# Kernel tuning notes

Measured on AMD Instinct MI355X. Metric: run time of the kernel, lower is better.

## Reference

```python
import jax, jax.numpy as jnp
import numpy as np

DIM = 512
HEADS = 8
DH = DIM // HEADS          # 64
M = DIM // 2               # 256 landmarks
PINV_ITERS = 6
KERNEL = 33                # residual_conv_kernel (lucidrains default)
SCALE = DH ** -0.5
LN_EPS = 1e-5


def setup_inputs() -> dict:
    key = jax.random.key(0)
    ks = jax.random.split(key, 6)
    b, n = 4, 4096
    x = jax.random.normal(ks[0], (b, n, DIM), jnp.float32)
    ln_w = jnp.ones((DIM,), jnp.float32)
    ln_b = jnp.zeros((DIM,), jnp.float32)
    w_qkv = jax.random.normal(ks[1], (DIM, 3 * DIM), jnp.float32) / np.float32(np.sqrt(DIM))
    w_out = jax.random.normal(ks[2], (DIM, DIM), jnp.float32) / np.float32(np.sqrt(DIM))
    b_out = jnp.zeros((DIM,), jnp.float32)
    # depthwise Conv2d(heads, heads, (33,1), groups=heads, bias=False): OIHW = (8,1,33,1)
    conv_w = jax.random.normal(ks[3], (HEADS, 1, KERNEL, 1), jnp.float32) / np.float32(np.sqrt(KERNEL))
    # admin_torch.as_module(8): residual x*omega + f(x), omega learnable scalar init sqrt(8)
    omega = jnp.asarray(np.sqrt(8.0), jnp.float32)
    return dict(x=x, ln_w=ln_w, ln_b=ln_b, w_qkv=w_qkv, w_out=w_out,
                b_out=b_out, conv_w=conv_w, omega=omega)


def _layernorm(x, w, b):
    mu = x.mean(-1, keepdims=True)
    var = x.var(-1, keepdims=True)
    return (x - mu) * jax.lax.rsqrt(var + LN_EPS) * w + b


def _moore_penrose_pinv(x, iters):
    # Newton-Schulz iteration, exactly as lucidrains nystrom-attention
    abs_x = jnp.abs(x)
    col = abs_x.sum(-1)
    row = abs_x.sum(-2)
    z = jnp.swapaxes(x, -1, -2) / (jnp.max(col) * jnp.max(row))
    I = jnp.eye(x.shape[-1], dtype=x.dtype)
    for _ in range(iters):
        xz = x @ z
        z = 0.25 * z @ (13. * I - xz @ (15. * I - xz @ (7. * I - xz)))
    return z


def reference(x, ln_w, ln_b, w_qkv, w_out, b_out, conv_w, omega):
    b, n, _ = x.shape
    nx = _layernorm(x, ln_w, ln_b)
    qkv = nx @ w_qkv                                # [b, n, 3*dim]
    q, k, v = jnp.split(qkv, 3, axis=-1)
    to_heads = lambda t: t.reshape(b, n, HEADS, DH).transpose(0, 2, 1, 3)  # bhnd
    q = to_heads(q) * SCALE
    k = to_heads(k)
    v = to_heads(v)
    l = n // M                                      # tokens per landmark group
    q_l = q.reshape(b, HEADS, M, l, DH).mean(3)     # [b,h,m,d]
    k_l = k.reshape(b, HEADS, M, l, DH).mean(3)
    sim1 = jnp.einsum('bhid,bhjd->bhij', q, k_l)    # [b,h,n,m]
    sim2 = jnp.einsum('bhid,bhjd->bhij', q_l, k_l)  # [b,h,m,m]
    sim3 = jnp.einsum('bhid,bhjd->bhij', q_l, k)    # [b,h,m,n]
    a1 = jax.nn.softmax(sim1, -1)
    a2 = jax.nn.softmax(sim2, -1)
    a3 = jax.nn.softmax(sim3, -1)
    a2_inv = _moore_penrose_pinv(a2, PINV_ITERS)
    out = (a1 @ a2_inv) @ (a3 @ v)                  # [b,h,n,d]
    # residual depthwise conv along the sequence dim of v
    res = jax.lax.conv_general_dilated(
        v, conv_w, window_strides=(1, 1),
        padding=((KERNEL // 2, KERNEL // 2), (0, 0)),
        dimension_numbers=('NCHW', 'OIHW', 'NCHW'),
        feature_group_count=HEADS)
    out = out + res
    out = out.transpose(0, 2, 1, 3).reshape(b, n, HEADS * DH)
    out = out @ w_out + b_out                       # to_out (dropout is eval no-op)
    return x * omega + out                          # admin residual
```

## Files before the change

kernel.cpp:

```cpp
#include <hip/hip_runtime.h>
#include <math.h>

#define B_    4
#define N_    4096
#define DIM_  512
#define H_    8
#define DH_   64
#define M_    256
#define LGRP  16
#define BH_   (B_*H_)
#define SCALE_ 0.125f
#define LN_EPS_ 1e-5f

#define SZ_QKVH (B_*H_*N_*DH_)
#define SZ_LM   (BH_*M_*DH_)
#define SZ_MM   (BH_*M_*M_)

typedef unsigned short ushort_t;
typedef __attribute__((ext_vector_type(8))) short bfrag8;
typedef __attribute__((ext_vector_type(4))) float fvec4;

__device__ __forceinline__ ushort_t f2b(float f) {
    unsigned u = __float_as_uint(f);
    unsigned r = (u + 0x7fffu + ((u >> 16) & 1u)) >> 16;
    return (ushort_t)r;
}
__device__ __forceinline__ float b2f(ushort_t s) {
    return __uint_as_float(((unsigned)s) << 16);
}

__device__ __forceinline__ void gload16(const ushort_t* g, ushort_t* l) {
    __builtin_amdgcn_global_load_lds(
        (const __attribute__((address_space(1))) void*)g,
        (__attribute__((address_space(3))) void*)l, 16, 0, 0);
}

__global__ __launch_bounds__(256) void ln_kernel(const float* __restrict__ x,
                                                 const float* __restrict__ w,
                                                 const float* __restrict__ bb,
                                                 ushort_t* __restrict__ nxb) {
    int row = blockIdx.x;
    int t = threadIdx.x;
    const float* xr = x + (size_t)row * DIM_;
    float v0 = xr[t], v1 = xr[t + 256];
    float s = v0 + v1, sq = v0 * v0 + v1 * v1;
    __shared__ float ls[4], lq[4];
    for (int off = 32; off > 0; off >>= 1) {
        s  += __shfl_down(s, off);
        sq += __shfl_down(sq, off);
    }
    int wid = t >> 6, lid = t & 63;
    if (lid == 0) { ls[wid] = s; lq[wid] = sq; }
    __syncthreads();
    if (t == 0) {
        float S = 0, Q = 0;
        for (int i = 0; i < 4; i++) { S += ls[i]; Q += lq[i]; }
        ls[0] = S; lq[0] = Q;
    }
    __syncthreads();
    float mean = ls[0] * (1.f / DIM_);
    float var  = lq[0] * (1.f / DIM_) - mean * mean;
    float rs = rsqrtf(var + LN_EPS_);
    ushort_t* o = nxb + (size_t)row * DIM_;
    o[t]       = f2b((v0 - mean) * rs * w[t]       + bb[t]);
    o[t + 256] = f2b((v1 - mean) * rs * w[t + 256] + bb[t + 256]);
}

__global__ __launch_bounds__(256) void tcast(const float* __restrict__ in,
                                             ushort_t* __restrict__ outT,
                                             int R, int C) {
    __shared__ float tile[32][33];
    int c0 = blockIdx.x * 32, r0 = blockIdx.y * 32;
    int t = threadIdx.x;
    #pragma unroll
    for (int u = 0; u < 4; u++) {
        int lin = t + 256 * u;
        int r = lin >> 5, c = lin & 31;
        tile[r][c] = in[(size_t)(r0 + r) * C + c0 + c];
    }
    __syncthreads();
    #pragma unroll
    for (int u = 0; u < 4; u++) {
        int lin = t + 256 * u;
        int cc = lin >> 5, rr = lin & 31;
        outT[(size_t)(c0 + cc) * R + r0 + rr] = f2b(tile[rr][cc]);
    }
}

template<int EPI>
__global__ __launch_bounds__(256) void gemm_bt128(const ushort_t* __restrict__ A,
                                                  const ushort_t* __restrict__ BT,
                                                  ushort_t* __restrict__ qb,
                                                  ushort_t* __restrict__ kb,
                                                  ushort_t* __restrict__ vb,
                                                  const float* __restrict__ x,
                                                  const float* __restrict__ bo,
                                                  const float* __restrict__ omega,
                                                  float* __restrict__ out) {
    const int K = 512;
    __shared__ __align__(16) ushort_t smem[4 * 128 * 64];
    int t = threadIdx.x;
    int lin = blockIdx.x + blockIdx.y * gridDim.x;
    int nwg = gridDim.x * gridDim.y;
    int wg  = (lin & 7) * (nwg >> 3) + (lin >> 3);
    int n0 = (wg % gridDim.x) * 128, m0 = (wg / gridDim.x) * 128;
    int w = t >> 6, lane = t & 63;
    int wr = (w >> 1) * 64, wc = (w & 1) * 64;
    int l15 = lane & 15, quad = lane >> 4, kq = quad * 8;
    int lrow = lane >> 3, lc8 = (lane & 7) * 8;
    int scol = lc8 ^ ((lrow & 7) << 3);
    int sw   = (l15 & 7) << 3;
    fvec4 acc[4][4] = {};

    auto stage = [&](int buf, int kc) {
        ushort_t* Ad = smem + buf * 16384;
        ushort_t* Bd = Ad + 8192;
        #pragma unroll
        for (int u = 0; u < 4; u++) {
            int r0 = (w << 5) + (u << 3);
            int row = r0 + lrow;
            const ushort_t* ga;
            if (EPI == 0) {
                ga = A + (size_t)(m0 + row) * K + kc + scol;
            } else {
                int grow = m0 + row; int b_ = grow >> 12, nn = grow & 4095;
                ga = A + (((size_t)(b_ * H_ + (kc >> 6)) * N_ + nn) << 6) + scol;
            }
            gload16(ga, Ad + r0 * 64);
            gload16(BT + (size_t)(n0 + row) * K + kc + scol, Bd + r0 * 64);
        }
    };

    stage(0, 0);
    __syncthreads();
    int cur = 0;
    for (int kt = 0; kt < 8; ++kt) {
        if (kt < 7) stage(cur ^ 1, (kt + 1) * 64);
        const ushort_t* As = smem + cur * 16384;
        const ushort_t* Bs = As + 8192;
        #pragma unroll
        for (int ks = 0; ks < 64; ks += 32) {
            int kcol = (ks + kq) ^ sw;
            bfrag8 a[4], b[4];
            #pragma unroll
            for (int r = 0; r < 4; r++) a[r] = *(bfrag8*)(As + (wr + r * 16 + l15) * 64 + kcol);
            #pragma unroll
            for (int c = 0; c < 4; c++) b[c] = *(bfrag8*)(Bs + (wc + c * 16 + l15) * 64 + kcol);
            #pragma unroll
            for (int r = 0; r < 4; r++)
                #pragma unroll
                for (int c = 0; c < 4; c++)
                    acc[r][c] = __builtin_amdgcn_mfma_f32_16x16x32_bf16(a[r], b[c], acc[r][c], 0, 0, 0);
        }
        __syncthreads();
        cur ^= 1;
    }

    if (EPI == 0) {
        int sec = n0 >> 9;
        float mul = (sec == 0) ? SCALE_ : 1.0f;
        ushort_t (*Ct)[132] = (ushort_t(*)[132])smem;
        #pragma unroll
        for (int r = 0; r < 4; r++) {
            #pragma unroll
            for (int reg = 0; reg < 4; reg++) {
                int lr = wr + r * 16 + quad * 4 + reg;
                #pragma unroll
                for (int c = 0; c < 4; c++) {
                    int lc = wc + c * 16 + l15;
                    Ct[lr][lc] = f2b(acc[r][c][reg] * mul);
                }
            }
        }
        __syncthreads();
        int row = t & 127, half = t >> 7;
        int grow = m0 + row; int b_ = grow >> 12, nn = grow & 4095;
        int head = ((n0 & 511) >> 6) + half;
        ushort_t* dstbuf = (sec == 0) ? qb : ((sec == 1) ? kb : vb);
        ushort_t* dp = dstbuf + (((size_t)(b_ * H_ + head) * N_ + nn) << 6);
        #pragma unroll
        for (int i = 0; i < 8; i++)
            *(uint4*)(dp + i * 8) = *(uint4*)&Ct[row][half * 64 + i * 8];
    } else {
        float om = omega[0];
        #pragma unroll
        for (int r = 0; r < 4; r++) {
            #pragma unroll
            for (int reg = 0; reg < 4; reg++) {
                int grow = m0 + wr + r * 16 + quad * 4 + reg;
                #pragma unroll
                for (int c = 0; c < 4; c++) {
                    int gcol = n0 + wc + c * 16 + l15;
                    size_t o = (size_t)grow * DIM_ + gcol;
                    out[o] = om * x[o] + bo[gcol] + acc[r][c][reg];
                }
            }
        }
    }
}

__global__ __launch_bounds__(256) void landmark_kernel(const ushort_t* __restrict__ q,
                                                       const ushort_t* __restrict__ k,
                                                       ushort_t* __restrict__ ql,
                                                       ushort_t* __restrict__ kl) {
    int idx = blockIdx.x * 256 + threadIdx.x;
    const ushort_t* src = blockIdx.y ? k : q;
    ushort_t* dst = blockIdx.y ? kl : ql;
    int d8 = (idx & 7) * 8;
    int m = (idx >> 3) & 255;
    int bh = idx >> 11;
    const ushort_t* p = src + (((size_t)bh * N_) + m * LGRP) * DH_ + d8;
    float s[8] = {};
    #pragma unroll
    for (int j = 0; j < LGRP; j++) {
        union { uint4 u4; ushort_t sv[8]; } val;
        val.u4 = *(const uint4*)(p + (size_t)j * DH_);
        #pragma unroll
        for (int e = 0; e < 8; e++) s[e] += b2f(val.sv[e]);
    }
    union { uint4 u4; ushort_t sv[8]; } o;
    #pragma unroll
    for (int e = 0; e < 8; e++) o.sv[e] = f2b(s[e] * (1.f / LGRP));
    *(uint4*)(dst + ((size_t)bh * M_ + m) * DH_ + d8) = o.u4;
}

__global__ __launch_bounds__(256) void sim2_softmax(const ushort_t* __restrict__ ql,
                                                    const ushort_t* __restrict__ kl,
                                                    float* __restrict__ a2,
                                                    ushort_t* __restrict__ a2b) {
    int i = blockIdx.x, bh = blockIdx.y, j = threadIdx.x;
    __shared__ float qrow[64];
    __shared__ float red[256];
    if (j < 64) qrow[j] = b2f(ql[((size_t)bh * M_ + i) * DH_ + j]);
    __syncthreads();
    const ushort_t* kr = kl + ((size_t)bh * M_ + j) * DH_;
    float s = 0;
    #pragma unroll
    for (int d = 0; d < 64; d++) s += qrow[d] * b2f(kr[d]);
    red[j] = s; __syncthreads();
    for (int off = 128; off > 0; off >>= 1) {
        if (j < off) red[j] = fmaxf(red[j], red[j + off]);
        __syncthreads();
    }
    float mx = red[0]; __syncthreads();
    float p = __expf(s - mx);
    red[j] = p; __syncthreads();
    for (int off = 128; off > 0; off >>= 1) {
        if (j < off) red[j] += red[j + off];
        __syncthreads();
    }
    float res = p / red[0];
    size_t o = ((size_t)bh * M_ + i) * M_ + j;
    a2[o] = res;
    a2b[o] = f2b(res);
}

__global__ void zero2(unsigned* p) { if (threadIdx.x < 2) p[threadIdx.x] = 0u; }

__global__ __launch_bounds__(256) void colpart(const float* __restrict__ a2,
                                               float* __restrict__ cs2) {
    int bh = blockIdx.x, s = blockIdx.y, t = threadIdx.x;
    const float* A = a2 + ((size_t)bh << 16) + (size_t)s * 32 * M_;
    float cs = 0.f;
    #pragma unroll
    for (int i = 0; i < 32; i++) cs += A[(size_t)i * M_ + t];
    cs2[((size_t)s * BH_ + bh) * M_ + t] = cs;
}

__global__ __launch_bounds__(256) void colmax(const float* __restrict__ cs2, unsigned* red) {
    int bh = blockIdx.x, t = threadIdx.x;
    float v = 0.f;
    #pragma unroll
    for (int s = 0; s < 8; s++) v += cs2[((size_t)s * BH_ + bh) * M_ + t];
    __shared__ float lr[256];
    lr[t] = v; __syncthreads();
    for (int off = 128; off > 0; off >>= 1) {
        if (t < off) lr[t] = fmaxf(lr[t], lr[t + off]);
        __syncthreads();
    }
    if (t == 0) atomicMax(red, __float_as_uint(lr[0]));
}

__global__ __launch_bounds__(256) void pinv_init2(const float* __restrict__ a2,
                                                  const unsigned* __restrict__ red,
                                                  ushort_t* __restrict__ zA,
                                                  ushort_t* __restrict__ zAT) {
    __shared__ float tile[32][33];
    int bt = blockIdx.z; int j0 = blockIdx.x * 32, i0 = blockIdx.y * 32;
    float invd = 1.f / __uint_as_float(red[0]);
    const float* Ab = a2 + ((size_t)bt << 16);
    size_t bo = (size_t)bt << 16;
    int t = threadIdx.x;
    #pragma unroll
    for (int u = 0; u < 4; u++) {
        int lin = t + 256 * u; int r = lin >> 5, c = lin & 31;
        float vv = Ab[(size_t)(i0 + r) * M_ + j0 + c] * invd;
        tile[r][c] = vv;
        zAT[bo + (size_t)(i0 + r) * M_ + j0 + c] = f2b(vv);
    }
    __syncthreads();
    #pragma unroll
    for (int u = 0; u < 4; u++) {
        int lin = t + 256 * u; int cc = lin >> 5, rr = lin & 31;
        zA[bo + (size_t)(j0 + cc) * M_ + i0 + rr] = f2b(tile[rr][cc]);
    }
}

__global__ __launch_bounds__(256) void gemm_pinv(const ushort_t* __restrict__ A,
                                                 const ushort_t* __restrict__ BT,
                                                 ushort_t* __restrict__ outN,
                                                 ushort_t* __restrict__ outT,
                                                 ushort_t* __restrict__ outT1,
                                                 float* __restrict__ outF,
                                                 float coefI, float scale) {
    __shared__ __align__(16) ushort_t smem[2 * 8192];
    int t = threadIdx.x;
    int lin = blockIdx.x + (blockIdx.y << 2) + (blockIdx.z << 4);
    int wg  = (lin & 7) * 64 + (lin >> 3);
    int n0 = (wg & 3) * 64, m0 = ((wg >> 2) & 3) * 64;
    int bt = wg >> 4;
    const ushort_t* Ab = A + ((size_t)bt << 16);
    const ushort_t* Bb = BT + ((size_t)bt << 16);
    int w = t >> 6, lane = t & 63;
    int wr = (w >> 1) * 32, wc = (w & 1) * 32;
    int l15 = lane & 15, quad = lane >> 4, kq = quad * 8;
    int lrow = lane >> 3, lc8 = (lane & 7) * 8;
    int scol = lc8 ^ ((lrow & 7) << 3);
    int sw   = (l15 & 7) << 3;
    fvec4 acc[2][2] = {};

    auto stage = [&](int buf, int kc) {
        ushort_t* Ad = smem + buf * 8192;
        ushort_t* Bd = Ad + 4096;
        #pragma unroll
        for (int u = 0; u < 2; u++) {
            int r0 = (w << 4) + (u << 3);
            int row = r0 + lrow;
            gload16(Ab + (size_t)(m0 + row) * M_ + kc + scol, Ad + r0 * 64);
            gload16(Bb + (size_t)(n0 + row) * M_ + kc + scol, Bd + r0 * 64);
        }
    };

    stage(0, 0);
    __syncthreads();
    int cur = 0;
    for (int kt = 0; kt < 4; ++kt) {
        if (kt < 3) stage(cur ^ 1, (kt + 1) * 64);
        const ushort_t* As = smem + cur * 8192;
        const ushort_t* Bs = As + 4096;
        #pragma unroll
        for (int ks = 0; ks < 64; ks += 32) {
            int kcol = (ks + kq) ^ sw;
            bfrag8 a[2], b[2];
            #pragma unroll
            for (int r = 0; r < 2; r++) a[r] = *(bfrag8*)(As + (wr + r * 16 + l15) * 64 + kcol);
            #pragma unroll
            for (int c = 0; c < 2; c++) b[c] = *(bfrag8*)(Bs + (wc + c * 16 + l15) * 64 + kcol);
            #pragma unroll
            for (int r = 0; r < 2; r++)
                #pragma unroll
                for (int c = 0; c < 2; c++)
                    acc[r][c] = __builtin_amdgcn_mfma_f32_16x16x32_bf16(a[r], b[c], acc[r][c], 0, 0, 0);
        }
        __syncthreads();
        cur ^= 1;
    }

    size_t bto = (size_t)bt << 16;
    if (outN || outF) {
        #pragma unroll
        for (int r = 0; r < 2; r++) {
            #pragma unroll
            for (int reg = 0; reg < 4; reg++) {
                int grow = m0 + wr + r * 16 + quad * 4 + reg;
                #pragma unroll
                for (int c = 0; c < 2; c++) {
                    int gcol = n0 + wc + c * 16 + l15;
                    float cv = scale * acc[r][c][reg] + (grow == gcol ? coefI : 0.f);
                    if (outN) outN[bto + (size_t)grow * M_ + gcol] = f2b(cv);
                    if (outF) outF[bto + (size_t)grow * M_ + gcol] = cv;
                }
            }
        }
    }
    if (outT || outT1) {
        ushort_t (*Ct)[65] = (ushort_t(*)[65])&smem[0];
        #pragma unroll
        for (int r = 0; r < 2; r++) {
            #pragma unroll
            for (int reg = 0; reg < 4; reg++) {
                int lr = wr + r * 16 + quad * 4 + reg;
                #pragma unroll
                for (int c = 0; c < 2; c++) {
                    int lc = wc + c * 16 + l15;
                    float cv = scale * acc[r][c][reg] + ((m0 + lr) == (n0 + lc) ? coefI : 0.f);
                    Ct[lr][lc] = f2b(cv);
                }
            }
        }
        __syncthreads();
        int j = t & 63, quarter = t >> 6, i0 = quarter * 16;
        #pragma unroll
        for (int vq = 0; vq < 2; vq++) {
            union { uint4 u4; ushort_t s[8]; } o1, o2;
            #pragma unroll
            for (int e = 0; e < 8; e++) {
                int il = i0 + vq * 8 + e;
                ushort_t bv = Ct[il][j];
                o1.s[e] = bv;
                o2.s[e] = f2b(((m0 + il) == (n0 + j) ? 7.f : 0.f) - b2f(bv));
            }
            size_t dst = bto + (size_t)(n0 + j) * M_ + m0 + i0 + vq * 8;
            if (outT)  *(uint4*)&outT[dst]  = o1.u4;
            if (outT1) *(uint4*)&outT1[dst] = o2.u4;
        }
    }
}

template<int NCH, int TRANSV>
__global__ __launch_bounds__(256) void flash_mfma(const ushort_t* __restrict__ Q,
                                                  const ushort_t* __restrict__ K,
                                                  const ushort_t* __restrict__ V,
                                                  ushort_t* __restrict__ Obf,
                                                  float* __restrict__ Opart,
                                                  float* __restrict__ lout,
                                                  int nq, int nk) {
    int bh = blockIdx.y;
    int nqt = nq >> 6;
    int qt = blockIdx.x % nqt;
    int ch = blockIdx.x / nqt;
    int q0 = qt * 64;
    int chunk = nk / NCH;
    int j0 = ch * chunk, j1 = j0 + chunk;

    __shared__ __align__(16) ushort_t qs[64][72];
    __shared__ __align__(16) ushort_t ks[64][72];
    __shared__ __align__(16) ushort_t vts[64][72];
    __shared__ __align__(16) ushort_t pb[64][72];

    int t = threadIdx.x;
    int w = t >> 6, lane = t & 63;
    int l15 = lane & 15, quad = lane >> 4, kq = quad * 8;
    int wrow = w * 16;

    const ushort_t* Qb = Q + ((size_t)bh * nq + q0) * DH_;
    #pragma unroll
    for (int u = 0; u < 2; u++) {
        int lin = t + 256 * u;
        int r = lin >> 3, cc = (lin & 7) * 8;
        *(uint4*)&qs[r][cc] = *(const uint4*)(Qb + r * DH_ + cc);
    }

    fvec4 Oacc[4];
    #pragma unroll
    for (int nt = 0; nt < 4; nt++)
        #pragma unroll
        for (int reg = 0; reg < 4; reg++) Oacc[nt][reg] = 0.f;
    float l_[4] = {0.f, 0.f, 0.f, 0.f};

    const ushort_t* VTbase = V + (size_t)bh * DH_ * nk;

    uint4 kreg[2], vreg[2];
    auto loadkv = [&](int j) {
        const ushort_t* Kb = K + ((size_t)bh * nk + j) * DH_;
        #pragma unroll
        for (int u = 0; u < 2; u++) {
            int lin = t + 256 * u;
            int r = lin >> 3, cc = (lin & 7) * 8;
            kreg[u] = *(const uint4*)(Kb + r * DH_ + cc);
            if (TRANSV == 0)
                vreg[u] = *(const uint4*)(VTbase + (size_t)r * nk + j + cc);
            else
                vreg[u] = *(const uint4*)(V + ((size_t)(bh * nk + j + r)) * DH_ + cc);
        }
    };
    auto writekv = [&]() {
        #pragma unroll
        for (int u = 0; u < 2; u++) {
            int lin = t + 256 * u;
            int r = lin >> 3, cc = (lin & 7) * 8;
            *(uint4*)&ks[r][cc] = kreg[u];
            if (TRANSV == 0) {
                *(uint4*)&vts[r][cc] = vreg[u];
            } else {
                union { uint4 u4; ushort_t s[8]; } vv;
                vv.u4 = vreg[u];
                #pragma unroll
                for (int m = 0; m < 8; m++) vts[cc + m][r] = vv.s[m];
            }
        }
    };

    loadkv(j0);
    for (int j = j0; j < j1; j += 64) {
        writekv();
        __syncthreads();
        if (j + 64 < j1) loadkv(j + 64);

        fvec4 S[4];
        #pragma unroll
        for (int ct = 0; ct < 4; ct++)
            #pragma unroll
            for (int reg = 0; reg < 4; reg++) S[ct][reg] = 0.f;
        bfrag8 aq0 = *(bfrag8*)&qs[wrow + l15][kq];
        bfrag8 aq1 = *(bfrag8*)&qs[wrow + l15][32 + kq];
        #pragma unroll
        for (int ct = 0; ct < 4; ct++) {
            bfrag8 b0 = *(bfrag8*)&ks[ct * 16 + l15][kq];
            bfrag8 b1 = *(bfrag8*)&ks[ct * 16 + l15][32 + kq];
            S[ct] = __builtin_amdgcn_mfma_f32_16x16x32_bf16(aq0, b0, S[ct], 0, 0, 0);
            S[ct] = __builtin_amdgcn_mfma_f32_16x16x32_bf16(aq1, b1, S[ct], 0, 0, 0);
        }

        float ps[4] = {0.f, 0.f, 0.f, 0.f};
        #pragma unroll
        for (int ct = 0; ct < 4; ct++) {
            #pragma unroll
            for (int reg = 0; reg < 4; reg++) {
                float pv = __expf(S[ct][reg]);
                ps[reg] += pv;
                pb[wrow + quad * 4 + reg][ct * 16 + l15] = f2b(pv);
            }
        }
        #pragma unroll
        for (int reg = 0; reg < 4; reg++) {
            float s = ps[reg];
            s += __shfl_xor(s, 1);
            s += __shfl_xor(s, 2);
            s += __shfl_xor(s, 4);
            s += __shfl_xor(s, 8);
            l_[reg] += s;
        }

        bfrag8 ap0 = *(bfrag8*)&pb[wrow + l15][kq];
        bfrag8 ap1 = *(bfrag8*)&pb[wrow + l15][32 + kq];
        #pragma unroll
        for (int nt = 0; nt < 4; nt++) {
            bfrag8 b0 = *(bfrag8*)&vts[nt * 16 + l15][kq];
            bfrag8 b1 = *(bfrag8*)&vts[nt * 16 + l15][32 + kq];
            Oacc[nt] = __builtin_amdgcn_mfma_f32_16x16x32_bf16(ap0, b0, Oacc[nt], 0, 0, 0);
            Oacc[nt] = __builtin_amdgcn_mfma_f32_16x16x32_bf16(ap1, b1, Oacc[nt], 0, 0, 0);
        }
        __syncthreads();
    }

    if (NCH == 1) {
        #pragma unroll
        for (int reg = 0; reg < 4; reg++) {
            float inv = 1.f / l_[reg];
            #pragma unroll
            for (int nt = 0; nt < 4; nt++)
                qs[wrow + quad * 4 + reg][nt * 16 + l15] = f2b(Oacc[nt][reg] * inv);
        }
        __syncthreads();
        ushort_t* Ob = Obf + ((size_t)bh * nq + q0) * DH_;
        #pragma unroll
        for (int u = 0; u < 2; u++) {
            int lin = t + 256 * u;
            int r = lin >> 3, i = (lin & 7) * 8;
            *(uint4*)(Ob + (size_t)r * DH_ + i) = *(uint4*)&qs[r][i];
        }
    } else {
        float (*Of)[68] = (float(*)[68])&ks[0][0];
        #pragma unroll
        for (int reg = 0; reg < 4; reg++)
            #pragma unroll
            for (int nt = 0; nt < 4; nt++)
                Of[wrow + quad * 4 + reg][nt * 16 + l15] = Oacc[nt][reg];
        size_t rows_per_ch = (size_t)BH_ * nq;
        size_t rowbase = (size_t)ch * rows_per_ch + (size_t)bh * nq + q0;
        if (l15 == 0) {
            #pragma unroll
            for (int reg = 0; reg < 4; reg++)
                lout[rowbase + wrow + quad * 4 + reg] = l_[reg];
        }
        __syncthreads();
        int orow = t >> 2, oc = (t & 3) * 16;
        float* Od = Opart + (rowbase + orow) * DH_ + oc;
        #pragma unroll
        for (int i = 0; i < 4; i++) {
            float4 v4 = make_float4(Of[orow][oc + i * 4], Of[orow][oc + i * 4 + 1],
                                    Of[orow][oc + i * 4 + 2], Of[orow][oc + i * 4 + 3]);
            *(float4*)(Od + i * 4) = v4;
        }
    }
}

__global__ __launch_bounds__(256) void flash_combine(const float* __restrict__ apart,
                                                     const float* __restrict__ lpart,
                                                     ushort_t* __restrict__ a3vb) {
    int idx = blockIdx.x * 256 + threadIdx.x;
    int d = idx & 63; int row = idx >> 6;
    const int R = BH_ * M_;
    size_t e = (size_t)row * DH_ + d;
    const size_t CH = (size_t)R * DH_;
    float l = 0.f, o = 0.f;
    #pragma unroll
    for (int s = 0; s < 8; s++) {
        l += lpart[row + (size_t)s * R];
        o += apart[e + (size_t)s * CH];
    }
    a3vb[e] = f2b(o / l);
}

__global__ __launch_bounds__(256) void wm_mfma(const ushort_t* __restrict__ Z,
                                               const ushort_t* __restrict__ A3V,
                                               ushort_t* __restrict__ WmT) {
    __shared__ __align__(16) ushort_t As[64][72];
    __shared__ __align__(16) ushort_t Bs[64][72];
    int bh = blockIdx.y;
    int i0 = blockIdx.x * 64;
    const ushort_t* Zb = Z + ((size_t)bh << 16);
    const ushort_t* Ab = A3V + ((size_t)bh << 14);
    int t = threadIdx.x;
    int w = t >> 6, lane = t & 63;
    int wr = (w >> 1) * 32, wc = (w & 1) * 32;
    int l15 = lane & 15, quad = lane >> 4, kq = quad * 8;
    fvec4 acc[2][2] = {};
    int rbase = t >> 3, c8 = (t & 7) * 8;

    for (int kc = 0; kc < M_; kc += 64) {
        #pragma unroll
        for (int u = 0; u < 2; u++) {
            int rr = rbase + 32 * u;
            *(float4*)&Bs[rr][c8] = *(const float4*)(Zb + (size_t)(i0 + rr) * M_ + kc + c8);
            union { uint4 u4; ushort_t s[8]; } av;
            av.u4 = *(const uint4*)(Ab + (size_t)(kc + rr) * DH_ + c8);
            #pragma unroll
            for (int m = 0; m < 8; m++) As[c8 + m][rr] = av.s[m];
        }
        __syncthreads();
        #pragma unroll
        for (int ks = 0; ks < 64; ks += 32) {
            bfrag8 a[2], b[2];
            #pragma unroll
            for (int r = 0; r < 2; r++) a[r] = *(bfrag8*)&As[wr + r * 16 + l15][ks + kq];
            #pragma unroll
            for (int c = 0; c < 2; c++) b[c] = *(bfrag8*)&Bs[wc + c * 16 + l15][ks + kq];
            #pragma unroll
            for (int r = 0; r < 2; r++)
                #pragma unroll
                for (int c = 0; c < 2; c++)
                    acc[r][c] = __builtin_amdgcn_mfma_f32_16x16x32_bf16(a[r], b[c], acc[r][c], 0, 0, 0);
        }
        __syncthreads();
    }
    #pragma unroll
    for (int r = 0; r < 2; r++) {
        #pragma unroll
        for (int reg = 0; reg < 4; reg++) {
            int drow = wr + r * 16 + quad * 4 + reg;
            ushort_t* dp = WmT + ((size_t)bh * DH_ + drow) * M_;
            #pragma unroll
            for (int c = 0; c < 2; c++)
                dp[i0 + wc + c * 16 + l15] = f2b(acc[r][c][reg]);
        }
    }
}

__global__ __launch_bounds__(256) void conv_kernel(const ushort_t* __restrict__ V,
                                                   const float* __restrict__ cw,
                                                   const ushort_t* __restrict__ ctxb,
                                                   ushort_t* __restrict__ outb) {
    int bh = blockIdx.y;
    int h = bh & 7;
    int i0 = blockIdx.x * 64;
    __shared__ float vb[96][64];
    __shared__ float wloc[33];
    int t = threadIdx.x;
    if (t < 33) wloc[t] = cw[h * 33 + t];
    #pragma unroll
    for (int u = 0; u < 3; u++) {
        int lin = t + 256 * u;
        int r = lin >> 3, cc = (lin & 7) * 8;
        int gi = i0 - 16 + r;
        union { uint4 u4; ushort_t s[8]; } val;
        if (gi >= 0 && gi < N_)
            val.u4 = *(const uint4*)(V + ((size_t)bh * N_ + gi) * DH_ + cc);
        else
            val.u4 = make_uint4(0, 0, 0, 0);
        #pragma unroll
        for (int m = 0; m < 8; m++) vb[r][cc + m] = b2f(val.s[m]);
    }
    __syncthreads();
    int d = t & 63, rb = t >> 6;
    for (int u = 0; u < 16; u++) {
        int r = rb * 16 + u;
        float s = 0.f;
        #pragma unroll
        for (int kk = 0; kk < 33; kk++) s += wloc[kk] * vb[r + kk][d];
        size_t o = ((size_t)bh * N_ + i0 + r) * DH_ + d;
        outb[o] = f2b(b2f(ctxb[o]) + s);
    }
}

extern "C" void kernel_launch(void* const* d_in, const int* in_sizes, int n_in,
                              void* d_out, int out_size, void* d_ws, size_t ws_size,
                              hipStream_t stream) {
    const float* x      = (const float*)d_in[0];
    const float* ln_w   = (const float*)d_in[1];
    const float* ln_b   = (const float*)d_in[2];
    const float* w_qkv  = (const float*)d_in[3];
    const float* w_out  = (const float*)d_in[4];
    const float* b_out  = (const float*)d_in[5];
    const float* conv_w = (const float*)d_in[6];
    const float* omega  = (const float*)d_in[7];
    float* out = (float*)d_out;

    float* fp = (float*)d_ws;
    float* a2    = fp;              fp += SZ_MM;
    float* apart = fp;              fp += SZ_QKVH / 2;
    float* lpart = fp;              fp += 8 * BH_ * M_;
    float* cs2   = fp;              fp += 8 * BH_ * M_;
    ushort_t* us = (ushort_t*)fp;
    ushort_t* wqkvT = us;           us += DIM_ * 3 * DIM_;
    ushort_t* woT   = us;           us += DIM_ * DIM_;
    ushort_t* a2b   = us;           us += SZ_MM;
    ushort_t* zA    = us;           us += SZ_MM;
    ushort_t* zAT   = us;           us += SZ_MM;
    ushort_t* zB    = us;           us += SZ_MM;
    ushort_t* zBT   = us;           us += SZ_MM;
    ushort_t* qb    = us;           us += SZ_QKVH;
    ushort_t* kb    = us;           us += SZ_QKVH;
    ushort_t* vb    = us;           us += SZ_QKVH;
    ushort_t* ctxb  = us;           us += SZ_QKVH;
    ushort_t* outhb = us;           us += SZ_QKVH;
    ushort_t* ql    = us;           us += SZ_LM;
    ushort_t* kl    = us;           us += SZ_LM;
    ushort_t* WmT   = us;           us += SZ_LM;
    ushort_t* a3vb  = us;           us += SZ_LM;
    unsigned* red   = (unsigned*)us;
    ushort_t* nxb = outhb;
    ushort_t* xz  = ctxb;
    ushort_t* t1T = xz  + SZ_MM;
    ushort_t* t2T = t1T + SZ_MM;
    ushort_t* t3T = t2T + SZ_MM;

    ln_kernel<<<B_ * N_, 256, 0, stream>>>(x, ln_w, ln_b, nxb);
    tcast<<<dim3(48, 16), 256, 0, stream>>>(w_qkv, wqkvT, DIM_, 3 * DIM_);
    tcast<<<dim3(16, 16), 256, 0, stream>>>(w_out, woT, DIM_, DIM_);
    gemm_bt128<0><<<dim3(12, 128), 256, 0, stream>>>(nxb, wqkvT, qb, kb, vb,
                                                     nullptr, nullptr, nullptr, nullptr);
    landmark_kernel<<<dim3(256, 2), 256, 0, stream>>>(qb, kb, ql, kl);
    sim2_softmax<<<dim3(M_, BH_), 256, 0, stream>>>(ql, kl, a2, a2b);
    zero2<<<1, 64, 0, stream>>>(red);
    colpart<<<dim3(BH_, 8), 256, 0, stream>>>(a2, cs2);
    colmax<<<BH_, 256, 0, stream>>>(cs2, red);
    pinv_init2<<<dim3(8, 8, 32), 256, 0, stream>>>(a2, red, zA, zAT);

    ushort_t* za = zA;  ushort_t* zaT = zAT;
    ushort_t* zb = zB;  ushort_t* zbT = zBT;
    for (int it = 0; it < 6; it++) {
        gemm_pinv<<<dim3(4, 4, BH_), 256, 0, stream>>>(a2b, zaT, xz, nullptr, t1T, nullptr, 0.f, 1.f);
        gemm_pinv<<<dim3(4, 4, BH_), 256, 0, stream>>>(xz, t1T, nullptr, t2T, nullptr, nullptr, 15.f, -1.f);
        gemm_pinv<<<dim3(4, 4, BH_), 256, 0, stream>>>(xz, t2T, nullptr, t3T, nullptr, nullptr, 13.f, -1.f);
        gemm_pinv<<<dim3(4, 4, BH_), 256, 0, stream>>>(za, t3T, zb, (it < 5) ? zbT : nullptr,
                                                       nullptr, nullptr, 0.f, 0.25f);
        ushort_t* tp;
        tp = za; za = zb; zb = tp;
        tp = zaT; zaT = zbT; zbT = tp;
    }

    flash_mfma<8, 1><<<dim3(32, BH_), 256, 0, stream>>>(ql, kb, vb, nullptr, apart, lpart, M_, N_);
    flash_combine<<<(BH_ * M_ * DH_) / 256, 256, 0, stream>>>(apart, lpart, a3vb);
    wm_mfma<<<dim3(4, BH_), 256, 0, stream>>>(za, a3vb, WmT);
    flash_mfma<1, 0><<<dim3(64, BH_), 256, 0, stream>>>(qb, kl, WmT, ctxb, nullptr, nullptr, N_, M_);
    conv_kernel<<<dim3(N_ / 64, BH_), 256, 0, stream>>>(vb, conv_w, ctxb, outhb);
    gemm_bt128<1><<<dim3(4, 128), 256, 0, stream>>>(outhb, woT, nullptr, nullptr, nullptr,
                                                    x, b_out, omega, out);
}
```

Measured before the change: 501.3 us.

## Add 256-row flash kernel for sim1 path and halve a3 split-K partitions

Adds a flash_big kernel in which each block handles 256 query rows against the 256 landmark keys. Each loaded K/WmT tile is reused across four 64-row sub-tiles, the next tile is prefetched into registers, and exp is applied without max subtraction. The a3·v flash pass drops from 8 split partitions to 4, shrinking the partial buffers and the combine work. The trade-off is fewer blocks (less parallelism) and more registers per thread, plus a softmax without running max that depends on scores staying bounded.

```diff
diff --git a/kernel.cpp b/kernel.cpp
--- a/kernel.cpp
+++ b/kernel.cpp
@@ -596,11 +596,148 @@
     const size_t CH = (size_t)R * DH_;
     float l = 0.f, o = 0.f;
     #pragma unroll
-    for (int s = 0; s < 8; s++) {
+    for (int s = 0; s < 4; s++) {
         l += lpart[row + (size_t)s * R];
         o += apart[e + (size_t)s * CH];
     }
     a3vb[e] = f2b(o / l);
+}
+
+__global__ __launch_bounds__(256) void flash_big(const ushort_t* __restrict__ Q,
+                                                 const ushort_t* __restrict__ K,
+                                                 const ushort_t* __restrict__ VT,
+                                                 ushort_t* __restrict__ Obf) {
+    const int nq = N_, nk = M_;
+    int bh = blockIdx.y;
+    int q0 = blockIdx.x * 256;
+    __shared__ __align__(16) ushort_t ks[64][72];
+    __shared__ __align__(16) ushort_t vts[64][72];
+    __shared__ __align__(16) ushort_t pb[2][64][72];
+
+    int t = threadIdx.x;
+    int w = t >> 6, lane = t & 63;
+    int l15 = lane & 15, quad = lane >> 4, kq = quad * 8;
+    int wrow = w * 16;
+
+    bfrag8 aq[4][2];
+    const ushort_t* Qb = Q + ((size_t)bh * nq + q0) * DH_;
+    #pragma unroll
+    for (int s = 0; s < 4; s++) {
+        #pragma unroll
+        for (int u = 0; u < 2; u++) {
+            int lin = t + 256 * u;
+            int r = lin >> 3, cc = (lin & 7) * 8;
+            *(uint4*)&pb[0][r][cc] = *(const uint4*)(Qb + (size_t)(s * 64 + r) * DH_ + cc);
+        }
+        __syncthreads();
+        aq[s][0] = *(bfrag8*)&pb[0][wrow + l15][kq];
+        aq[s][1] = *(bfrag8*)&pb[0][wrow + l15][32 + kq];
+        __syncthreads();
+    }
+
+    fvec4 Oacc[4][4];
+    #pragma unroll
+    for (int s = 0; s < 4; s++)
+        #pragma unroll
+        for (int nt = 0; nt < 4; nt++)
+            #pragma unroll
+            for (int reg = 0; reg < 4; reg++) Oacc[s][nt][reg] = 0.f;
+    float l_[4][4];
+    #pragma unroll
+    for (int s = 0; s < 4; s++)
+        #pragma unroll
+        for (int reg = 0; reg < 4; reg++) l_[s][reg] = 0.f;
+
+    const ushort_t* VTb = VT + (size_t)bh * DH_ * nk;
+    uint4 kreg[2], vreg[2];
+    auto loadkv = [&](int j) {
+        const ushort_t* Kb = K + ((size_t)bh * nk + j) * DH_;
+        #pragma unroll
+        for (int u = 0; u < 2; u++) {
+            int lin = t + 256 * u;
+            int r = lin >> 3, cc = (lin & 7) * 8;
+            kreg[u] = *(const uint4*)(Kb + (size_t)r * DH_ + cc);
+            vreg[u] = *(const uint4*)(VTb + (size_t)r * nk + j + cc);
+        }
+    };
+
+    loadkv(0);
+    for (int j = 0; j < nk; j += 64) {
+        #pragma unroll
+        for (int u = 0; u < 2; u++) {
+            int lin = t + 256 * u;
+            int r = lin >> 3, cc = (lin & 7) * 8;
+            *(uint4*)&ks[r][cc] = kreg[u];
+            *(uint4*)&vts[r][cc] = vreg[u];
+        }
+        __syncthreads();
+        if (j + 64 < nk) loadkv(j + 64);
+
+        #pragma unroll
+        for (int s = 0; s < 4; s++) {
+            fvec4 S[4];
+            #pragma unroll
+            for (int ct = 0; ct < 4; ct++)
+                #pragma unroll
+                for (int reg = 0; reg < 4; reg++) S[ct][reg] = 0.f;
+            #pragma unroll
+            for (int ct = 0; ct < 4; ct++) {
+                bfrag8 b0 = *(bfrag8*)&ks[ct * 16 + l15][kq];
+                bfrag8 b1 = *(bfrag8*)&ks[ct * 16 + l15][32 + kq];
+                S[ct] = __builtin_amdgcn_mfma_f32_16x16x32_bf16(aq[s][0], b0, S[ct], 0, 0, 0);
+                S[ct] = __builtin_amdgcn_mfma_f32_16x16x32_bf16(aq[s][1], b1, S[ct], 0, 0, 0);
+            }
+            float ps[4] = {0.f, 0.f, 0.f, 0.f};
+            #pragma unroll
+            for (int ct = 0; ct < 4; ct++) {
+                #pragma unroll
+                for (int reg = 0; reg < 4; reg++) {
+                    float pv = __expf(S[ct][reg]);
+                    ps[reg] += pv;
+                    pb[s & 1][wrow + quad * 4 + reg][ct * 16 + l15] = f2b(pv);
+                }
+            }
+            #pragma unroll
+            for (int reg = 0; reg < 4; reg++) {
+                float sm = ps[reg];
+                sm += __shfl_xor(sm, 1);
+                sm += __shfl_xor(sm, 2);
+                sm += __shfl_xor(sm, 4);
+                sm += __shfl_xor(sm, 8);
+                l_[s][reg] += sm;
+            }
+            bfrag8 ap0 = *(bfrag8*)&pb[s & 1][wrow + l15][kq];
+            bfrag8 ap1 = *(bfrag8*)&pb[s & 1][wrow + l15][32 + kq];
+            #pragma unroll
+            for (int nt = 0; nt < 4; nt++) {
+                bfrag8 v0 = *(bfrag8*)&vts[nt * 16 + l15][kq];
+                bfrag8 v1 = *(bfrag8*)&vts[nt * 16 + l15][32 + kq];
+                Oacc[s][nt] = __builtin_amdgcn_mfma_f32_16x16x32_bf16(ap0, v0, Oacc[s][nt], 0, 0, 0);
+                Oacc[s][nt] = __builtin_amdgcn_mfma_f32_16x16x32_bf16(ap1, v1, Oacc[s][nt], 0, 0, 0);
+            }
+        }
+        __syncthreads();
+    }
+
+    ushort_t* Ob = Obf + ((size_t)bh * nq + q0) * DH_;
+    #pragma unroll
+    for (int s = 0; s < 4; s++) {
+        #pragma unroll
+        for (int reg = 0; reg < 4; reg++) {
+            float inv = 1.f / l_[s][reg];
+            #pragma unroll
+            for (int nt = 0; nt < 4; nt++)
+                pb[0][wrow + quad * 4 + reg][nt * 16 + l15] = f2b(Oacc[s][nt][reg] * inv);
+        }
+        __syncthreads();
+        #pragma unroll
+        for (int u = 0; u < 2; u++) {
+            int lin = t + 256 * u;
+            int r = lin >> 3, i = (lin & 7) * 8;
+            *(uint4*)(Ob + (size_t)(s * 64 + r) * DH_ + i) = *(uint4*)&pb[0][r][i];
+        }
+        __syncthreads();
+    }
 }
 
 __global__ __launch_bounds__(256) void wm_mfma(const ushort_t* __restrict__ Z,
@@ -709,8 +846,8 @@
 
     float* fp = (float*)d_ws;
     float* a2    = fp;              fp += SZ_MM;
-    float* apart = fp;              fp += SZ_QKVH / 2;
-    float* lpart = fp;              fp += 8 * BH_ * M_;
+    float* apart = fp;              fp += SZ_QKVH / 4;
+    float* lpart = fp;              fp += 4 * BH_ * M_;
     float* cs2   = fp;              fp += 8 * BH_ * M_;
     ushort_t* us = (ushort_t*)fp;
     ushort_t* wqkvT = us;           us += DIM_ * 3 * DIM_;
@@ -761,10 +898,10 @@
         tp = zaT; zaT = zbT; zbT = tp;
     }
 
-    flash_mfma<8, 1><<<dim3(32, BH_), 256, 0, stream>>>(ql, kb, vb, nullptr, apart, lpart, M_, N_);
+    flash_mfma<4, 1><<<dim3(16, BH_), 256, 0, stream>>>(ql, kb, vb, nullptr, apart, lpart, M_, N_);
     flash_combine<<<(BH_ * M_ * DH_) / 256, 256, 0, stream>>>(apart, lpart, a3vb);
     wm_mfma<<<dim3(4, BH_), 256, 0, stream>>>(za, a3vb, WmT);
-    flash_mfma<1, 0><<<dim3(64, BH_), 256, 0, stream>>>(qb, kl, WmT, ctxb, nullptr, nullptr, N_, M_);
+    flash_big<<<dim3(N_ / 256, BH_), 256, 0, stream>>>(qb, kl, WmT, ctxb);
     conv_kernel<<<dim3(N_ / 64, BH_), 256, 0, stream>>>(vb, conv_w, ctxb, outhb);
     gemm_bt128<1><<<dim3(4, 128), 256, 0, stream>>>(outhb, woT, nullptr, nullptr, nullptr,
                                                     x, b_out, omega, out);
```

After: 488.0 us. -2.7%, faster.
